# Optimization experiments

Hardware: AMD Instinct MI355X
Metric: run time of the kernel (lower is better)

The kernel has to match this reference:

```python
import jax, jax.numpy as jnp
import numpy as np

N_FFT = 254
WIN = 254
HOP = 64
ITERS = 50
AUDIO_DIM = 16384
MAX_VALUE = 69.37411499023438


def _hann(n):
    # tf.signal.hann_window (periodic)
    return (0.5 - 0.5 * jnp.cos(2.0 * jnp.pi * jnp.arange(n) / n)).astype(jnp.float32)


def _synth_window():
    # tf.signal.inverse_stft_window_fn(HOP) applied to hann forward window
    w = _hann(WIN)
    overlaps = -(-WIN // HOP)
    d = jnp.pad(w * w, (0, overlaps * HOP - WIN))
    d = d.reshape(overlaps, HOP).sum(axis=0)  # overlap-added squared window per phase
    d = jnp.tile(d, overlaps)[:WIN]
    return w / d


def _stft(x, window):
    # x: [B, L] -> [B, F, N_FFT//2+1]; win_length == n_fft so no zero-padding of frames
    L = x.shape[1]
    nf = 1 + (L - WIN) // HOP
    idx = jnp.arange(nf)[:, None] * HOP + jnp.arange(WIN)
    frames = x[:, idx] * window
    return jnp.fft.rfft(frames, n=N_FFT)


def _istft(spec, swin, out_len):
    # spec: [B, F, bins] -> [B, out_len] via windowed overlap-add
    frames = jnp.fft.irfft(spec, n=N_FFT)[..., :WIN] * swin
    nf = frames.shape[1]
    idx = jnp.arange(nf)[:, None] * HOP + jnp.arange(WIN)
    out = jnp.zeros((frames.shape[0], out_len), frames.dtype)
    return out.at[:, idx].add(frames)


def setup_inputs() -> dict:
    key = jax.random.key(0)
    x = jax.random.uniform(key, (128, 256, 128, 1), dtype=jnp.float32)
    return {"x": x}


def reference(x):
    win = _hann(WIN)
    swin = _synth_window()
    # de-log / de-normalize the spectrogram
    mag = jnp.exp(5.0 * (x - 1.0)) * MAX_VALUE
    mag = jnp.squeeze(mag, -1)  # [B, F, 128]
    nframes = mag.shape[1]
    out_len = HOP * (nframes - 1) + WIN  # 16574

    # Griffin-Lim: initial reconstruction with zero phase
    waveform = _istft(mag.astype(jnp.complex64), swin, out_len)

    def step(wf, _):
        phase = jnp.angle(_stft(wf, win))
        spec = mag * jnp.exp(1j * phase)
        return _istft(spec, swin, out_len), None

    waveform, _ = jax.lax.scan(step, waveform, None, length=ITERS)

    waveform = waveform / jnp.max(jnp.abs(waveform))
    return waveform[:, :AUDIO_DIM, None]  # [B, 16384, 1]
```

## Files before the change

kernel.cpp:

```cpp
#include <hip/hip_runtime.h>
#include <math.h>


#define B_SZ 128
#define NFRM 256
#define BINS 128
#define NFFT 254
#define OUTL 16574
#define AUD  16384
#define GL_ITERS 50
#define MAXV 69.37411499023438f
#define PI2f 6.2831853071795864f

typedef __attribute__((ext_vector_type(8))) short short8;
typedef __attribute__((ext_vector_type(4))) short short4v;
typedef __attribute__((ext_vector_type(4))) float f32x4;

__device__ __forceinline__ unsigned short f2bf(float f) {
  unsigned u = __float_as_uint(f);
  return (unsigned short)((u + 0x7FFFu + ((u >> 16) & 1u)) >> 16);
}
__device__ __forceinline__ float bf2f(unsigned short h) {
  return __uint_as_float(((unsigned)h) << 16);
}
__device__ __forceinline__ void split3(float v, short* h, short* m, short* l) {
  unsigned short hh = f2bf(v);
  float r1 = v - bf2f(hh);
  unsigned short mm = f2bf(r1);
  float r2 = r1 - bf2f(mm);
  *h = (short)hh; *m = (short)mm; *l = (short)f2bf(r2);
}
__device__ __forceinline__ int slotf(int c, int row) {
  return (c & ~7) | ((c ^ row ^ (row >> 3)) & 7);
}

#define MFMA6(ACC, AH, AM, AL, BH, BM, BL)                                   \
  ACC = __builtin_amdgcn_mfma_f32_16x16x32_bf16(AH, BL, ACC, 0, 0, 0);       \
  ACC = __builtin_amdgcn_mfma_f32_16x16x32_bf16(AM, BM, ACC, 0, 0, 0);       \
  ACC = __builtin_amdgcn_mfma_f32_16x16x32_bf16(AL, BH, ACC, 0, 0, 0);       \
  ACC = __builtin_amdgcn_mfma_f32_16x16x32_bf16(AH, BM, ACC, 0, 0, 0);       \
  ACC = __builtin_amdgcn_mfma_f32_16x16x32_bf16(AM, BH, ACC, 0, 0, 0);       \
  ACC = __builtin_amdgcn_mfma_f32_16x16x32_bf16(AH, BH, ACC, 0, 0, 0);

__global__ void tables_k(short* __restrict__ WfH, short* __restrict__ WfM,
                         short* __restrict__ WfL, short* __restrict__ CI,
                         short* __restrict__ SI, float* __restrict__ swin,
                         unsigned* __restrict__ gmax) {
  int tid = blockIdx.x * blockDim.x + threadIdx.x;
  if (tid == 0) *gmax = 0u;
  if (tid < 256) {
    float v = 0.f;
    if (tid < NFFT) {
      float wn = 0.5f - 0.5f * cosf(PI2f * (float)tid / (float)NFFT);
      float d = 0.f;
      int p = tid & 63;
      for (int q = 0; q < 4; ++q) {
        int nn = p + 64 * q;
        if (nn < NFFT) { float w = 0.5f - 0.5f * cosf(PI2f * (float)nn / (float)NFFT); d += w * w; }
      }
      v = wn / d;
    }
    swin[tid] = v;
  }
  if (tid < 65536) {
    int j = tid & 7, l = (tid >> 3) & 63, nt = (tid >> 9) & 15, kc = tid >> 13;
    int krow = kc * 32 + ((l >> 4) << 3) + j;
    int ncol = (nt << 4) + (l & 15);
    float v1 = 0.f;
    if (krow < NFFT) {
      int kk = ncol >> 1;
      int m = (kk * krow) % NFFT;
      float ang = PI2f * (float)m / (float)NFFT;
      float wn = 0.5f - 0.5f * cosf(PI2f * (float)krow / (float)NFFT);
      v1 = wn * ((ncol & 1) ? -sinf(ang) : cosf(ang));
    }
    split3(v1, &WfH[tid], &WfM[tid], &WfL[tid]);
  }
  if (tid < 16384) {
    int j = tid & 7, l = (tid >> 3) & 63;
    int krow = (tid >> 12) * 32 + ((l >> 4) << 3) + j;
    int ncol = (((tid >> 9) & 7) << 4) + (l & 15);
    int m = (krow * ncol) % NFFT;
    float ang = PI2f * (float)m / (float)NFFT;
    float sc = ((krow == 0 || krow == BINS - 1) ? 1.f : 2.f) / (float)NFFT;
    split3(sc * cosf(ang), &CI[tid], &CI[16384 + tid], &CI[32768 + tid]);
    split3(-sc * sinf(ang), &SI[tid], &SI[16384 + tid], &SI[32768 + tid]);
  }
}

__global__ void mag_k(const float* __restrict__ x, float* __restrict__ mag) {
  int i = blockIdx.x * 256 + threadIdx.x;
  mag[i] = expf(5.f * (x[i] - 1.f)) * MAXV;
}

template <int FIRST>
__global__ __launch_bounds__(512) void iter_k(
    const float* __restrict__ FRsrc, float* __restrict__ FRdst,
    const float* __restrict__ mag, const float* __restrict__ swin,
    const short* __restrict__ WfH, const short* __restrict__ WfM,
    const short* __restrict__ WfL,
    const short* __restrict__ CI, const short* __restrict__ SI) {
  __shared__ __align__(16) short Y[24576];
  __shared__ __align__(16) char scratch[16896];
  short* wfsH = (short*)scratch;
  short* wfsM = wfsH + 2240;
  short* wfsL = wfsM + 2240;
  float* trA = (float*)scratch;
  float* trB = trA + 2112;

  int o = blockIdx.x;
  int blk = ((o & 7) << 7) + (o >> 3);
  int b = blk >> 3, f0 = (blk & 7) << 5;
  int tid = threadIdx.x, lane = tid & 63, wv = tid >> 6;
  int fgl = b * NFRM + f0;

  if (FIRST) {
    int row = tid >> 4, q = tid & 15;
    int srow = fgl + row;
    float4 m0 = *(const float4*)&mag[((size_t)srow << 7) + (q << 3)];
    float4 m1 = *(const float4*)&mag[((size_t)srow << 7) + (q << 3) + 4];
    float mv[8] = {m0.x, m0.y, m0.z, m0.w, m1.x, m1.y, m1.z, m1.w};
    short h[8] __attribute__((aligned(16))), m[8] __attribute__((aligned(16))),
          l[8] __attribute__((aligned(16))), z[8] __attribute__((aligned(16)));
#pragma unroll
    for (int e = 0; e < 8; ++e) { split3(mv[e], &h[e], &m[e], &l[e]); z[e] = 0; }
    int off = (row << 7) + (slotf(q, row) << 3);
    *(short8*)&Y[off]         = *(const short8*)h;
    *(short8*)&Y[4096 + off]  = *(const short8*)m;
    *(short8*)&Y[8192 + off]  = *(const short8*)l;
    *(short8*)&Y[12288 + off] = *(const short8*)z;
    *(short8*)&Y[16384 + off] = *(const short8*)z;
    *(short8*)&Y[20480 + off] = *(const short8*)z;
  } else {
    const float* FRb = FRsrc + ((size_t)b << 16);
    for (int i4 = tid; i4 < 560; i4 += 512) {
      int i = i4 << 2;
      int t = (f0 << 6) + i;
      int ft = t >> 6, cb = t & 63;
      float4 s = make_float4(0.f, 0.f, 0.f, 0.f);
#pragma unroll
      for (int d = 3; d >= 0; --d) {
        int f = ft - d;
        if (f >= 0 && f <= 255) {
          float4 v = *(const float4*)&FRb[(f << 8) + cb + (d << 6)];
          s.x += v.x; s.y += v.y; s.z += v.z; s.w += v.w;
        }
      }
      if (i == 2236) { s.z = 0.f; s.w = 0.f; }
      short hh[4] __attribute__((aligned(8))), mm[4] __attribute__((aligned(8))),
            ll[4] __attribute__((aligned(8)));
      split3(s.x, &hh[0], &mm[0], &ll[0]);
      split3(s.y, &hh[1], &mm[1], &ll[1]);
      split3(s.z, &hh[2], &mm[2], &ll[2]);
      split3(s.w, &hh[3], &mm[3], &ll[3]);
      int q = i >> 3;
      int qs = (q & ~7) | ((q ^ (q >> 3)) & 7);
      int p = (qs << 3) | (i & 7);
      *(short4v*)&wfsH[p] = *(const short4v*)hh;
      *(short4v*)&wfsM[p] = *(const short4v*)mm;
      *(short4v*)&wfsL[p] = *(const short4v*)ll;
    }

    f32x4 acc1[2][2];
#pragma unroll
    for (int i = 0; i < 2; ++i) { acc1[i][0] = (f32x4){0,0,0,0}; acc1[i][1] = (f32x4){0,0,0,0}; }

    __syncthreads();

    for (int kc = 0; kc < 8; ++kc) {
      short8 Ah[2], Am[2], Al[2];
#pragma unroll
      for (int mt = 0; mt < 2; ++mt) {
        int frame = (mt << 4) + (lane & 15);
        int q = (frame << 3) + (kc << 2) + (lane >> 4);
        int qs = (q & ~7) | ((q ^ (q >> 3)) & 7);
        Ah[mt] = *(const short8*)&wfsH[qs << 3];
        Am[mt] = *(const short8*)&wfsM[qs << 3];
        Al[mt] = *(const short8*)&wfsL[qs << 3];
      }
#pragma unroll
      for (int nt = 0; nt < 2; ++nt) {
        int ntg = (wv << 1) + nt;
        size_t off = (((size_t)((kc << 4) + ntg) << 6) + lane) << 3;
        short8 bh = *(const short8*)(WfH + off);
        short8 bm = *(const short8*)(WfM + off);
        short8 bl = *(const short8*)(WfL + off);
        __builtin_amdgcn_s_setprio(1);
#pragma unroll
        for (int mt = 0; mt < 2; ++mt) {
          MFMA6(acc1[mt][nt], Ah[mt], Am[mt], Al[mt], bh, bm, bl)
        }
        __builtin_amdgcn_s_setprio(0);
      }
    }

    for (int mtg = 0; mtg < 2; ++mtg) {
      __syncthreads();
#pragma unroll
      for (int nt = 0; nt < 2; ++nt) {
        int col = (((wv << 1) + nt) << 4) | (lane & 15);
        int cc = col >> 3, hb = (col >> 2) & 1, w = col & 3;
        float* th = hb ? trB : trA;
        int base = (cc << 2) + w;
#pragma unroll
        for (int r = 0; r < 4; ++r) {
          int row16 = ((lane >> 4) << 2) + r;
          th[row16 * 132 + base] = acc1[mtg][nt][r];
        }
      }
      __syncthreads();
      {
        int trow = tid >> 5;
        int c = tid & 31;
        float4 va = *(const float4*)&trA[trow * 132 + (c << 2)];
        float4 vb = *(const float4*)&trB[trow * 132 + (c << 2)];
        int lrow = (mtg << 4) + trow;
        int srow = fgl + lrow;
        float4 xm = *(const float4*)&mag[((size_t)srow << 7) + (c << 2)];
        float vv[8] = {va.x, va.y, va.z, va.w, vb.x, vb.y, vb.z, vb.w};
        short reh[4] __attribute__((aligned(8))), rem[4] __attribute__((aligned(8))),
              rel[4] __attribute__((aligned(8))), imh[4] __attribute__((aligned(8))),
              imm[4] __attribute__((aligned(8))), iml[4] __attribute__((aligned(8)));
#pragma unroll
        for (int pq = 0; pq < 4; ++pq) {
          float mg = ((const float*)&xm)[pq];
          float re = vv[2 * pq], im = vv[2 * pq + 1];
          float s2 = re * re + im * im;
          float ore, oim;
          if (s2 == 0.f) { ore = mg; oim = 0.f; }
          else { float rr = mg * rsqrtf(s2); ore = re * rr; oim = im * rr; }
          split3(ore, &reh[pq], &rem[pq], &rel[pq]);
          split3(oim, &imh[pq], &imm[pq], &iml[pq]);
        }
        int c2 = c >> 1, half = (c & 1) << 2;
        int off2 = (lrow << 7) + (slotf(c2, lrow) << 3) + half;
        *(short4v*)&Y[off2]         = *(const short4v*)reh;
        *(short4v*)&Y[4096 + off2]  = *(const short4v*)rem;
        *(short4v*)&Y[8192 + off2]  = *(const short4v*)rel;
        *(short4v*)&Y[12288 + off2] = *(const short4v*)imh;
        *(short4v*)&Y[16384 + off2] = *(const short4v*)imm;
        *(short4v*)&Y[20480 + off2] = *(const short4v*)iml;
      }
    }
  }

  f32x4 aC[2], aS[2];
#pragma unroll
  for (int i = 0; i < 2; ++i) { aC[i] = (f32x4){0,0,0,0}; aS[i] = (f32x4){0,0,0,0}; }

  __syncthreads();

  for (int kc = 0; kc < 4; ++kc) {
    short8 ReH[2], ReM[2], ReL[2], ImH[2], ImM[2], ImL[2];
#pragma unroll
    for (int mt = 0; mt < 2; ++mt) {
      int rl = (mt << 4) + (lane & 15);
      int c = (kc << 2) + (lane >> 4);
      int off = (rl << 7) + (slotf(c, rl) << 3);
      ReH[mt] = *(const short8*)&Y[off];
      ReM[mt] = *(const short8*)&Y[4096 + off];
      ReL[mt] = *(const short8*)&Y[8192 + off];
      ImH[mt] = *(const short8*)&Y[12288 + off];
      ImM[mt] = *(const short8*)&Y[16384 + off];
      ImL[mt] = *(const short8*)&Y[20480 + off];
    }
    size_t flat = (((size_t)((kc << 3) + wv) << 6) + lane) << 3;
    short8 ch = *(const short8*)(CI + flat);
    short8 cm = *(const short8*)(CI + 16384 + flat);
    short8 cl = *(const short8*)(CI + 32768 + flat);
    short8 sh = *(const short8*)(SI + flat);
    short8 sm = *(const short8*)(SI + 16384 + flat);
    short8 sl = *(const short8*)(SI + 32768 + flat);
    __builtin_amdgcn_s_setprio(1);
#pragma unroll
    for (int mt = 0; mt < 2; ++mt) {
      MFMA6(aC[mt], ReH[mt], ReM[mt], ReL[mt], ch, cm, cl)
      MFMA6(aS[mt], ImH[mt], ImM[mt], ImL[mt], sh, sm, sl)
    }
    __builtin_amdgcn_s_setprio(0);
  }

  {
    int n = (wv << 4) + (lane & 15);
    float swn = swin[n];
    float swp = swin[254 - n];
    float* FRo = FRdst + ((size_t)b << 16) + ((size_t)f0 << 8);
#pragma unroll
    for (int mt = 0; mt < 2; ++mt)
#pragma unroll
      for (int r = 0; r < 4; ++r) {
        int row = (mt << 4) + ((lane >> 4) << 2) + r;
        float C = aC[mt][r], S_ = aS[mt][r];
        FRo[((size_t)row << 8) + n] = swn * (C + S_);
        if (n >= 1 && n <= 126) FRo[((size_t)row << 8) + 254 - n] = swp * (C - S_);
        if (n == 0) { FRo[((size_t)row << 8) + 254] = 0.f; FRo[((size_t)row << 8) + 255] = 0.f; }
      }
  }
}

__global__ void redmax_k(const float* __restrict__ FR, unsigned* __restrict__ gmax) {
  __shared__ float red[16];
  int b = blockIdx.x;
  const float* FRb = FR + ((size_t)b << 16);
  float v = 0.f;
  for (int t = threadIdx.x; t < OUTL; t += 1024) {
    int f_hi = t >> 6; if (f_hi > NFRM - 1) f_hi = NFRM - 1;
    int f_lo = (t >= NFFT) ? (((t - NFFT) >> 6) + 1) : 0;
    float s = 0.f;
    for (int f = f_lo; f <= f_hi; ++f) s += FRb[(f << 8) + t - (f << 6)];
    v = fmaxf(v, fabsf(s));
  }
#pragma unroll
  for (int o = 32; o > 0; o >>= 1) v = fmaxf(v, __shfl_xor(v, o, 64));
  if ((threadIdx.x & 63) == 0) red[threadIdx.x >> 6] = v;
  __syncthreads();
  if (threadIdx.x < 16) {
    v = red[threadIdx.x];
#pragma unroll
    for (int o = 8; o > 0; o >>= 1) v = fmaxf(v, __shfl_xor(v, o, 16));
    if (threadIdx.x == 0) atomicMax(gmax, __float_as_uint(v));
  }
}

__global__ void out_k(const float* __restrict__ FR, const unsigned* __restrict__ gmax,
                      float* __restrict__ out) {
  int b = blockIdx.y, t = blockIdx.x * 256 + threadIdx.x;
  const float* FRb = FR + ((size_t)b << 16);
  int f_hi = t >> 6; if (f_hi > NFRM - 1) f_hi = NFRM - 1;
  int f_lo = (t >= NFFT) ? (((t - NFFT) >> 6) + 1) : 0;
  float s = 0.f;
  for (int f = f_lo; f <= f_hi; ++f) s += FRb[(f << 8) + t - (f << 6)];
  float g = __uint_as_float(*gmax);
  out[(size_t)b * AUD + t] = s / g;
}

extern "C" void kernel_launch(void* const* d_in, const int* in_sizes, int n_in,
                              void* d_out, int out_size, void* d_ws, size_t ws_size,
                              hipStream_t stream) {
  const float* x = (const float*)d_in[0];

  float* FR0 = (float*)d_ws;
  float* FR1 = FR0 + 8388608;
  float* mag = FR1 + 8388608;
  short* WfH = (short*)(mag + 4194304);
  short* WfM = WfH + 65536;
  short* WfL = WfM + 65536;
  short* CI  = WfL + 65536;
  short* SI  = CI + 49152;
  float* swin = (float*)(SI + 49152);
  unsigned* gmax = (unsigned*)(swin + 256);

  mag_k<<<16384, 256, 0, stream>>>(x, mag);
  tables_k<<<256, 256, 0, stream>>>(WfH, WfM, WfL, CI, SI, swin, gmax);

  iter_k<1><<<1024, 512, 0, stream>>>(FR1, FR0, mag, swin, WfH, WfM, WfL, CI, SI);

  float* bufs[2] = {FR0, FR1};
  for (int it = 0; it < GL_ITERS; ++it) {
    iter_k<0><<<1024, 512, 0, stream>>>(bufs[it & 1], bufs[(it + 1) & 1], mag, swin,
                                        WfH, WfM, WfL, CI, SI);
  }

  redmax_k<<<B_SZ, 1024, 0, stream>>>(FR0, gmax);
  out_k<<<dim3(64, B_SZ), 256, 0, stream>>>(FR0, gmax, (float*)d_out);
}
```

Before: 2.109 ms.

## Stream phase-projection and inverse DFT per 32-bin chunk with double-buffered LDS

Replaces the full 32x128 spectrum staging buffer with a loop over four 32-bin chunks. Each chunk's forward-DFT accumulators are transposed through a small padded buffer, phase-normalized and bf16-split, then written into one of two ping-pong LDS buffers before the inverse-DFT MFMAs run on it. This shrinks LDS use, which may raise occupancy, and interleaves the projection with the MFMA work. The cost is more block-wide barriers, and only 256 of the 512 threads do the projection step.

```diff
diff --git a/kernel.cpp b/kernel.cpp
--- a/kernel.cpp
+++ b/kernel.cpp
@@ -29,9 +29,6 @@
   unsigned short mm = f2bf(r1);
   float r2 = r1 - bf2f(mm);
   *h = (short)hh; *m = (short)mm; *l = (short)f2bf(r2);
-}
-__device__ __forceinline__ int slotf(int c, int row) {
-  return (c & ~7) | ((c ^ row ^ (row >> 3)) & 7);
 }
 
 #define MFMA6(ACC, AH, AM, AL, BH, BM, BL)                                   \
@@ -100,13 +97,12 @@
     const short* __restrict__ WfH, const short* __restrict__ WfM,
     const short* __restrict__ WfL,
     const short* __restrict__ CI, const short* __restrict__ SI) {
-  __shared__ __align__(16) short Y[24576];
-  __shared__ __align__(16) char scratch[16896];
-  short* wfsH = (short*)scratch;
-  short* wfsM = wfsH + 2240;
-  short* wfsL = wfsM + 2240;
-  float* trA = (float*)scratch;
-  float* trB = trA + 2112;
+  __shared__ __align__(16) short wfsB[6720];
+  __shared__ __align__(16) float tr[2080];
+  __shared__ __align__(16) short Sc[12288];
+  short* wfsH = wfsB;
+  short* wfsM = wfsB + 2240;
+  short* wfsL = wfsB + 4480;
 
   int o = blockIdx.x;
   int blk = ((o & 7) << 7) + (o >> 3);
@@ -114,24 +110,12 @@
   int tid = threadIdx.x, lane = tid & 63, wv = tid >> 6;
   int fgl = b * NFRM + f0;
 
-  if (FIRST) {
-    int row = tid >> 4, q = tid & 15;
-    int srow = fgl + row;
-    float4 m0 = *(const float4*)&mag[((size_t)srow << 7) + (q << 3)];
-    float4 m1 = *(const float4*)&mag[((size_t)srow << 7) + (q << 3) + 4];
-    float mv[8] = {m0.x, m0.y, m0.z, m0.w, m1.x, m1.y, m1.z, m1.w};
-    short h[8] __attribute__((aligned(16))), m[8] __attribute__((aligned(16))),
-          l[8] __attribute__((aligned(16))), z[8] __attribute__((aligned(16)));
-#pragma unroll
-    for (int e = 0; e < 8; ++e) { split3(mv[e], &h[e], &m[e], &l[e]); z[e] = 0; }
-    int off = (row << 7) + (slotf(q, row) << 3);
-    *(short8*)&Y[off]         = *(const short8*)h;
-    *(short8*)&Y[4096 + off]  = *(const short8*)m;
-    *(short8*)&Y[8192 + off]  = *(const short8*)l;
-    *(short8*)&Y[12288 + off] = *(const short8*)z;
-    *(short8*)&Y[16384 + off] = *(const short8*)z;
-    *(short8*)&Y[20480 + off] = *(const short8*)z;
-  } else {
+  f32x4 acc1[2][2];
+  f32x4 aC[2], aS[2];
+#pragma unroll
+  for (int i = 0; i < 2; ++i) { aC[i] = (f32x4){0,0,0,0}; aS[i] = (f32x4){0,0,0,0}; }
+
+  if (!FIRST) {
     const float* FRb = FRsrc + ((size_t)b << 16);
     for (int i4 = tid; i4 < 560; i4 += 512) {
       int i = i4 << 2;
@@ -161,7 +145,6 @@
       *(short4v*)&wfsL[p] = *(const short4v*)ll;
     }
 
-    f32x4 acc1[2][2];
 #pragma unroll
     for (int i = 0; i < 2; ++i) { acc1[i][0] = (f32x4){0,0,0,0}; acc1[i][1] = (f32x4){0,0,0,0}; }
 
@@ -193,91 +176,92 @@
         __builtin_amdgcn_s_setprio(0);
       }
     }
-
-    for (int mtg = 0; mtg < 2; ++mtg) {
-      __syncthreads();
-#pragma unroll
-      for (int nt = 0; nt < 2; ++nt) {
-        int col = (((wv << 1) + nt) << 4) | (lane & 15);
-        int cc = col >> 3, hb = (col >> 2) & 1, w = col & 3;
-        float* th = hb ? trB : trA;
-        int base = (cc << 2) + w;
-#pragma unroll
-        for (int r = 0; r < 4; ++r) {
-          int row16 = ((lane >> 4) << 2) + r;
-          th[row16 * 132 + base] = acc1[mtg][nt][r];
+  }
+
+  for (int kb = 0; kb < 4; ++kb) {
+    int pofs = (kb & 1) * 6144;
+
+    if (!FIRST && (wv >> 1) == kb) {
+      int q = wv & 1;
+#pragma unroll
+      for (int mt = 0; mt < 2; ++mt)
+#pragma unroll
+        for (int nt = 0; nt < 2; ++nt) {
+          int cl = (q << 5) + (nt << 4) + (lane & 15);
+#pragma unroll
+          for (int r = 0; r < 4; ++r) {
+            int row = (mt << 4) + ((lane >> 4) << 2) + r;
+            tr[row * 65 + cl] = acc1[mt][nt][r];
+          }
         }
-      }
-      __syncthreads();
-      {
-        int trow = tid >> 5;
-        int c = tid & 31;
-        float4 va = *(const float4*)&trA[trow * 132 + (c << 2)];
-        float4 vb = *(const float4*)&trB[trow * 132 + (c << 2)];
-        int lrow = (mtg << 4) + trow;
-        int srow = fgl + lrow;
-        float4 xm = *(const float4*)&mag[((size_t)srow << 7) + (c << 2)];
-        float vv[8] = {va.x, va.y, va.z, va.w, vb.x, vb.y, vb.z, vb.w};
-        short reh[4] __attribute__((aligned(8))), rem[4] __attribute__((aligned(8))),
-              rel[4] __attribute__((aligned(8))), imh[4] __attribute__((aligned(8))),
-              imm[4] __attribute__((aligned(8))), iml[4] __attribute__((aligned(8)));
-#pragma unroll
-        for (int pq = 0; pq < 4; ++pq) {
-          float mg = ((const float*)&xm)[pq];
-          float re = vv[2 * pq], im = vv[2 * pq + 1];
+    }
+    __syncthreads();
+    if (tid < 256) {
+      int row = tid >> 3, c8 = tid & 7;
+      int srow = fgl + row;
+      float4 mg4 = *(const float4*)&mag[((size_t)srow << 7) + (kb << 5) + (c8 << 2)];
+      short reh[4] __attribute__((aligned(8))), rem[4] __attribute__((aligned(8))),
+            rel[4] __attribute__((aligned(8))), imh[4] __attribute__((aligned(8))),
+            imm[4] __attribute__((aligned(8))), iml[4] __attribute__((aligned(8)));
+#pragma unroll
+      for (int e = 0; e < 4; ++e) {
+        float mg = ((const float*)&mg4)[e];
+        float ore, oim;
+        if (FIRST) { ore = mg; oim = 0.f; }
+        else {
+          float re = tr[row * 65 + (c8 << 3) + 2 * e];
+          float im = tr[row * 65 + (c8 << 3) + 2 * e + 1];
           float s2 = re * re + im * im;
-          float ore, oim;
           if (s2 == 0.f) { ore = mg; oim = 0.f; }
           else { float rr = mg * rsqrtf(s2); ore = re * rr; oim = im * rr; }
-          split3(ore, &reh[pq], &rem[pq], &rel[pq]);
-          split3(oim, &imh[pq], &imm[pq], &iml[pq]);
         }
-        int c2 = c >> 1, half = (c & 1) << 2;
-        int off2 = (lrow << 7) + (slotf(c2, lrow) << 3) + half;
-        *(short4v*)&Y[off2]         = *(const short4v*)reh;
-        *(short4v*)&Y[4096 + off2]  = *(const short4v*)rem;
-        *(short4v*)&Y[8192 + off2]  = *(const short4v*)rel;
-        *(short4v*)&Y[12288 + off2] = *(const short4v*)imh;
-        *(short4v*)&Y[16384 + off2] = *(const short4v*)imm;
-        *(short4v*)&Y[20480 + off2] = *(const short4v*)iml;
-      }
-    }
-  }
-
-  f32x4 aC[2], aS[2];
-#pragma unroll
-  for (int i = 0; i < 2; ++i) { aC[i] = (f32x4){0,0,0,0}; aS[i] = (f32x4){0,0,0,0}; }
-
-  __syncthreads();
-
-  for (int kc = 0; kc < 4; ++kc) {
-    short8 ReH[2], ReM[2], ReL[2], ImH[2], ImM[2], ImL[2];
-#pragma unroll
-    for (int mt = 0; mt < 2; ++mt) {
-      int rl = (mt << 4) + (lane & 15);
-      int c = (kc << 2) + (lane >> 4);
-      int off = (rl << 7) + (slotf(c, rl) << 3);
-      ReH[mt] = *(const short8*)&Y[off];
-      ReM[mt] = *(const short8*)&Y[4096 + off];
-      ReL[mt] = *(const short8*)&Y[8192 + off];
-      ImH[mt] = *(const short8*)&Y[12288 + off];
-      ImM[mt] = *(const short8*)&Y[16384 + off];
-      ImL[mt] = *(const short8*)&Y[20480 + off];
-    }
-    size_t flat = (((size_t)((kc << 3) + wv) << 6) + lane) << 3;
-    short8 ch = *(const short8*)(CI + flat);
-    short8 cm = *(const short8*)(CI + 16384 + flat);
-    short8 cl = *(const short8*)(CI + 32768 + flat);
-    short8 sh = *(const short8*)(SI + flat);
-    short8 sm = *(const short8*)(SI + 16384 + flat);
-    short8 sl = *(const short8*)(SI + 32768 + flat);
-    __builtin_amdgcn_s_setprio(1);
-#pragma unroll
-    for (int mt = 0; mt < 2; ++mt) {
-      MFMA6(aC[mt], ReH[mt], ReM[mt], ReL[mt], ch, cm, cl)
-      MFMA6(aS[mt], ImH[mt], ImM[mt], ImL[mt], sh, sm, sl)
-    }
-    __builtin_amdgcn_s_setprio(0);
+        split3(ore, &reh[e], &rem[e], &rel[e]);
+        split3(oim, &imh[e], &imm[e], &iml[e]);
+      }
+      int cc = c8 >> 1, half = (c8 & 1) << 2;
+      int sre = (cc ^ row ^ (row >> 3)) & 7;
+      int sim = ((4 + cc) ^ row ^ (row >> 3)) & 7;
+      int are = (row << 6) + (sre << 3) + half;
+      int aim = (row << 6) + (sim << 3) + half;
+      *(short4v*)&Sc[pofs + are]        = *(const short4v*)reh;
+      *(short4v*)&Sc[pofs + aim]        = *(const short4v*)imh;
+      *(short4v*)&Sc[pofs + 2048 + are] = *(const short4v*)rem;
+      *(short4v*)&Sc[pofs + 2048 + aim] = *(const short4v*)imm;
+      *(short4v*)&Sc[pofs + 4096 + are] = *(const short4v*)rel;
+      *(short4v*)&Sc[pofs + 4096 + aim] = *(const short4v*)iml;
+    }
+    __syncthreads();
+
+    {
+      size_t flat = (((size_t)((kb << 3) + wv) << 6) + lane) << 3;
+      short8 ciH = *(const short8*)(CI + flat);
+      short8 ciM = *(const short8*)(CI + 16384 + flat);
+      short8 ciL = *(const short8*)(CI + 32768 + flat);
+      short8 siH = *(const short8*)(SI + flat);
+      short8 siM = *(const short8*)(SI + 16384 + flat);
+      short8 siL = *(const short8*)(SI + 32768 + flat);
+      short8 ReH[2], ReM[2], ReL[2], ImH[2], ImM[2], ImL[2];
+#pragma unroll
+      for (int mt = 0; mt < 2; ++mt) {
+        int row = (mt << 4) + (lane & 15);
+        int cr = lane >> 4;
+        int ar = (row << 6) + (((cr ^ row ^ (row >> 3)) & 7) << 3);
+        int ai = (row << 6) + ((((4 + cr) ^ row ^ (row >> 3)) & 7) << 3);
+        ReH[mt] = *(const short8*)&Sc[pofs + ar];
+        ImH[mt] = *(const short8*)&Sc[pofs + ai];
+        ReM[mt] = *(const short8*)&Sc[pofs + 2048 + ar];
+        ImM[mt] = *(const short8*)&Sc[pofs + 2048 + ai];
+        ReL[mt] = *(const short8*)&Sc[pofs + 4096 + ar];
+        ImL[mt] = *(const short8*)&Sc[pofs + 4096 + ai];
+      }
+      __builtin_amdgcn_s_setprio(1);
+#pragma unroll
+      for (int mt = 0; mt < 2; ++mt) {
+        MFMA6(aC[mt], ReH[mt], ReM[mt], ReL[mt], ciH, ciM, ciL)
+        MFMA6(aS[mt], ImH[mt], ImM[mt], ImL[mt], siH, siM, siL)
+      }
+      __builtin_amdgcn_s_setprio(0);
+    }
   }
 
   {
```

After: 2.802 ms. 1.33x slower.
